# Kernel tuning notes

Measured on AMD Instinct MI355X. Metric: run time of the kernel, lower is better.

Reference implementation:

```python
import jax, jax.numpy as jnp
import numpy as np

B, S, C = 32, 128, 32
VOCAB, E, H = 262, 128, 256


def _gru_dir(x_proj, mask, W_hh, b_hh, reverse):
    # x_proj: [C, N, 3H] time-major precomputed input projection
    # mask:   [C, N, 1]  1.0 where char is valid
    N = x_proj.shape[1]
    h0 = jnp.zeros((N, H), x_proj.dtype)

    def step(h, inp):
        x3, mt = inp
        gh = h @ W_hh.T + b_hh                      # [N, 3H]
        hr, hz, hn = jnp.split(gh, 3, axis=-1)
        xr, xz, xn = jnp.split(x3, 3, axis=-1)
        r = jax.nn.sigmoid(xr + hr)
        z = jax.nn.sigmoid(xz + hz)
        n = jnp.tanh(xn + r * hn)
        hnew = (1.0 - z) * n + z * h
        h = mt * hnew + (1.0 - mt) * h              # freeze state past seq end
        return h, None

    hT, _ = jax.lax.scan(step, h0, (x_proj, mask), reverse=reverse)
    return hT  # [N, H] final state at last valid step (fw) / step 0 (bw)


def char_rnn_forward(chars, chars_mask, data_mask, embed,
                     W_ih_fw, W_hh_fw, b_ih_fw, b_hh_fw,
                     W_ih_bw, W_hh_bw, b_ih_bw, b_hh_bw):
    b, s, c = chars.shape
    N = b * s
    x = embed[chars.reshape(N, c)]                      # [N, C, E]
    m = chars_mask.reshape(N, c).astype(x.dtype)        # [N, C]
    mm = jnp.moveaxis(m, 1, 0)[:, :, None]              # [C, N, 1]

    def run(W_ih, b_ih, W_hh, b_hh, reverse):
        xp = jnp.einsum('nce,ge->ncg', x, W_ih) + b_ih  # [N, C, 3H]
        xp = jnp.moveaxis(xp, 1, 0)                     # [C, N, 3H]
        return _gru_dir(xp, mm, W_hh, b_hh, reverse)

    h_fw = run(W_ih_fw, b_ih_fw, W_hh_fw, b_hh_fw, False)
    h_bw = run(W_ih_bw, b_ih_bw, W_hh_bw, b_hh_bw, True)
    final = jnp.concatenate([h_fw, h_bw], axis=-1).reshape(b, s, 2 * H)
    return final * data_mask[:, :, None].astype(final.dtype)


def setup_inputs() -> dict:
    key = jax.random.key(0)
    ks = jax.random.split(key, 16)
    chars = jax.random.randint(ks[0], (B, S, C), 0, VOCAB, dtype=jnp.int32)
    # ragged but contiguous lengths, as pack_padded_sequence assumes (>=1)
    word_len = jax.random.randint(ks[1], (B,), 1, S + 1)
    char_len = jax.random.randint(ks[2], (B, S), 1, C + 1)
    data_mask = (jnp.arange(S)[None, :] < word_len[:, None]).astype(jnp.int32)
    chars_mask = (jnp.arange(C)[None, None, :] < char_len[:, :, None]).astype(jnp.int32)
    chars_mask = chars_mask * data_mask[:, :, None]
    # pack_padded needs length>=1 even for padded words (torch never runs them;
    # we mask their output with data_mask, so give them 1 valid char)
    chars_mask = chars_mask.at[:, :, 0].set(1)

    sc = 1.0 / np.sqrt(H)
    def unif(k, shape):
        return jax.random.uniform(k, shape, jnp.float32, -sc, sc)
    embed = jax.random.normal(ks[3], (VOCAB, E), jnp.float32) * 0.1
    return {
        'chars': chars, 'chars_mask': chars_mask, 'data_mask': data_mask,
        'embed': embed,
        'W_ih_fw': unif(ks[4], (3 * H, E)), 'W_hh_fw': unif(ks[5], (3 * H, H)),
        'b_ih_fw': unif(ks[6], (3 * H,)),  'b_hh_fw': unif(ks[7], (3 * H,)),
        'W_ih_bw': unif(ks[8], (3 * H, E)), 'W_hh_bw': unif(ks[9], (3 * H, H)),
        'b_ih_bw': unif(ks[10], (3 * H,)), 'b_hh_bw': unif(ks[11], (3 * H,)),
    }


def reference(chars, chars_mask, data_mask, embed,
              W_ih_fw, W_hh_fw, b_ih_fw, b_hh_fw,
              W_ih_bw, W_hh_bw, b_ih_bw, b_hh_bw):
    return char_rnn_forward(chars, chars_mask, data_mask, embed,
                            W_ih_fw, W_hh_fw, b_ih_fw, b_hh_fw,
                            W_ih_bw, W_hh_bw, b_ih_bw, b_hh_bw)
```

## Files before the change

kernel.cpp:

```cpp
#include <hip/hip_runtime.h>
#include <hip/hip_bf16.h>

typedef unsigned int u32;
typedef unsigned short u16;
typedef __attribute__((ext_vector_type(8))) short bf16x8;
typedef __attribute__((ext_vector_type(4))) float f32x4;

#define NWORDS 4096
#define CC 32
#define EE 128
#define HHH 256
#define MMW 32
#define VOCABN 262

#define HS 272
#define XPS 784

#define PK_HHD (16*3*8*512)
#define XP_OFF_U16 (2*PK_HHD)
#define XPD (VOCABN*768)
#define BIAS_OFF_U16 (XP_OFF_U16 + 2*XPD)

__device__ __forceinline__ float bf2f(u16 u){ union{u32 i; float f;} v; v.i=((u32)u)<<16; return v.f; }
__device__ __forceinline__ u16 f2bf(float f){
  __hip_bfloat16 h = __float2bfloat16(f);
  u16 r; __builtin_memcpy(&r, &h, 2); return r;
}
__device__ __forceinline__ float sigmoid_f(float x){
  float e = __builtin_amdgcn_exp2f(-1.4426950408889634f * x);
  return __builtin_amdgcn_rcpf(1.0f + e);
}
__device__ __forceinline__ float tanh_f(float x){
  float ax = __builtin_fabsf(x);
  float e  = __builtin_amdgcn_exp2f(-2.8853900817779268f * ax);
  float t  = 1.0f - 2.0f * e * __builtin_amdgcn_rcpf(1.0f + e);
  return __builtin_copysignf(t, x);
}

__global__ void prep_pack(const float* __restrict__ Whh_fw, const float* __restrict__ Whh_bw,
                          u16* __restrict__ wsu)
{
  int idx = blockIdx.x*256 + threadIdx.x;
  int d = idx / PK_HHD;
  int e = idx - d*PK_HHD;
  const float* Whh = d ? Whh_bw : Whh_fw;
  int jj   = e & 7;
  int lane = (e >> 3) & 63;
  int kc   = (e >> 9) & 7;
  int gnt  = e >> 12;
  int g = gnt % 3, nt = gnt / 3;
  int row = g*256 + nt*16 + (lane & 15);
  int k   = kc*32 + ((lane >> 4) << 3) + jj;
  wsu[idx] = f2bf(Whh[row*HHH + k]);
}

__global__ void prep_xp(const float* __restrict__ emb,
                        const float* __restrict__ Wih_fw, const float* __restrict__ Wih_bw,
                        u16* __restrict__ wsu)
{
  int i = blockIdx.x*256 + threadIdx.x;
  int d = i / XPD;
  int r = i - d*XPD;
  int c = r / 768, g = r - c*768;
  const float* W = (d ? Wih_bw : Wih_fw) + g*EE;
  const float* E = emb + c*EE;
  float acc = 0.0f;
  #pragma unroll 4
  for (int e = 0; e < EE; e += 4) {
    float4 ev = *(const float4*)(E + e);
    float4 wv = *(const float4*)(W + e);
    acc = fmaf(ev.w, wv.w, fmaf(ev.z, wv.z, fmaf(ev.y, wv.y, fmaf(ev.x, wv.x, acc))));
  }
  wsu[XP_OFF_U16 + i] = f2bf(acc);
}

__global__ void prep_bias(const float* __restrict__ bih_fw, const float* __restrict__ bhh_fw,
                          const float* __restrict__ bih_bw, const float* __restrict__ bhh_bw,
                          u16* __restrict__ wsu)
{
  int i = blockIdx.x*256 + threadIdx.x;
  if (i >= 2048) return;
  int d = i >> 10, o = i & 1023;
  const float* bih = d ? bih_bw : bih_fw;
  const float* bhh = d ? bhh_bw : bhh_fw;
  float v;
  if (o < 512)      v = bih[o] + bhh[o];
  else if (o < 768) v = bih[o - 512 + 512];
  else              v = bhh[o - 768 + 512];
  ((float*)(wsu + BIAS_OFF_U16))[d*1024 + o] = v;
}

__global__ __launch_bounds__(1024)
void gru_mfma(const int* __restrict__ chars, const int* __restrict__ chars_mask,
              const int* __restrict__ data_mask, const u16* __restrict__ wsu,
              float* __restrict__ out)
{
  const int dir   = blockIdx.x & 1;
  const int word0 = (blockIdx.x >> 1) * MMW;
  const int j     = threadIdx.x;
  const int wave  = j >> 6, lane = j & 63;
  const int quad  = lane >> 4, l15 = lane & 15;

  const bf16x8* pHH  = (const bf16x8*)(wsu + (size_t)dir*PK_HHD);
  const u16*    xpt  = wsu + XP_OFF_U16 + (size_t)dir*XPD;
  const float*  bias = (const float*)(wsu + BIAS_OFF_U16) + dir*1024;

  const bf16x8* bHH = pHH + (size_t)(wave*3)*8*64 + lane;

  __shared__ __align__(16) u16   sh_hhi[MMW][HS];
  __shared__ __align__(16) u16   sh_hlo[MMW][HS];
  __shared__ __align__(16) u16   sh_xp[MMW][XPS];
  __shared__ float sh_m[MMW];

  for (int i = j; i < MMW*HS/2; i += 1024) { ((float*)sh_hhi)[i] = 0.0f; ((float*)sh_hlo)[i] = 0.0f; }

  const int ch = wave*16 + l15;
  const float bR  = bias[ch],        bZ  = bias[256 + ch];
  const float bXN = bias[512 + ch],  bHN = bias[768 + ch];

  const int sw = j >> 5, sp = j & 31;

  bf16x8 buf[4][3];
  auto load_batch = [&](int kc, bf16x8 dst[3]) {
    #pragma unroll
    for (int g = 0; g < 3; ++g) dst[g] = bHH[(g*8 + kc)*64];
  };
  load_batch(0, buf[0]);
  load_batch(1, buf[1]);
  load_batch(2, buf[2]);

  #pragma unroll 1
  for (int s = 0; s < CC; ++s) {
    const int t = dir ? (CC - 1 - s) : s;
    __syncthreads();
    {
      int ci = chars[(word0 + sw)*CC + t];
      const uint4* src = (const uint4*)(xpt + (size_t)ci*768);
      uint4 a0 = src[sp*3], a1 = src[sp*3+1], a2 = src[sp*3+2];
      *(uint4*)&sh_xp[sw][sp*24]      = a0;
      *(uint4*)&sh_xp[sw][sp*24 + 8]  = a1;
      *(uint4*)&sh_xp[sw][sp*24 + 16] = a2;
      if (j < MMW) sh_m[j] = (float)chars_mask[(word0 + j)*CC + t];
    }
    __syncthreads();

    f32x4 acc[3][2];
    #pragma unroll
    for (int m = 0; m < 2; ++m) {
      acc[0][m] = (f32x4){bR,bR,bR,bR};
      acc[1][m] = (f32x4){bZ,bZ,bZ,bZ};
      acc[2][m] = (f32x4){bHN,bHN,bHN,bHN};
    }

    auto mfma_batch = [&](int kc, bf16x8 src[3]) {
      #pragma unroll
      for (int m = 0; m < 2; ++m) {
        bf16x8 ah = *(const bf16x8*)&sh_hhi[m*16 + l15][kc*32 + quad*8];
        bf16x8 al = *(const bf16x8*)&sh_hlo[m*16 + l15][kc*32 + quad*8];
        #pragma unroll
        for (int g = 0; g < 3; ++g) {
          const int ai = (g < 2) ? g : 2;
          acc[ai][m] = __builtin_amdgcn_mfma_f32_16x16x32_bf16(ah, src[g], acc[ai][m], 0,0,0);
          acc[ai][m] = __builtin_amdgcn_mfma_f32_16x16x32_bf16(al, src[g], acc[ai][m], 0,0,0);
        }
      }
    };

    #pragma unroll
    for (int b = 0; b < 8; ++b) {
      mfma_batch(b, buf[b & 3]);
      load_batch((b + 3) & 7, buf[(b + 3) & 3]);
    }

    __syncthreads();

    #pragma unroll
    for (int m = 0; m < 2; ++m)
      #pragma unroll
      for (int r = 0; r < 4; ++r) {
        const int word = m*16 + quad*4 + r;
        float xr = bf2f(sh_xp[word][ch]);
        float xz = bf2f(sh_xp[word][256 + ch]);
        float xn = bf2f(sh_xp[word][512 + ch]);
        float rr = sigmoid_f(acc[0][m][r] + xr);
        float zz = sigmoid_f(acc[1][m][r] + xz);
        float nn = tanh_f(fmaf(rr, acc[2][m][r], bXN + xn));
        float hold = bf2f(sh_hhi[word][ch]) + bf2f(sh_hlo[word][ch]);
        float hnew = fmaf(zz, hold - nn, nn);
        float hm   = fmaf(sh_m[word], hnew - hold, hold);
        u16 hi = f2bf(hm);
        sh_hhi[word][ch] = hi;
        sh_hlo[word][ch] = f2bf(hm - bf2f(hi));
      }
  }
  __syncthreads();

  const int oc = j & 255, og = j >> 8;
  #pragma unroll
  for (int i = 0; i < 8; ++i) {
    const int w = og*8 + i;
    float dm = (float)data_mask[word0 + w];
    float h = bf2f(sh_hhi[w][oc]) + bf2f(sh_hlo[w][oc]);
    out[(size_t)(word0 + w)*(2*HHH) + dir*HHH + oc] = h * dm;
  }
}

extern "C" void kernel_launch(void* const* d_in, const int* in_sizes, int n_in,
                              void* d_out, int out_size, void* d_ws, size_t ws_size,
                              hipStream_t stream) {
  const int*   chars      = (const int*)d_in[0];
  const int*   chars_mask = (const int*)d_in[1];
  const int*   data_mask  = (const int*)d_in[2];
  const float* embed      = (const float*)d_in[3];
  const float* Wih_fw     = (const float*)d_in[4];
  const float* Whh_fw     = (const float*)d_in[5];
  const float* bih_fw     = (const float*)d_in[6];
  const float* bhh_fw     = (const float*)d_in[7];
  const float* Wih_bw     = (const float*)d_in[8];
  const float* Whh_bw     = (const float*)d_in[9];
  const float* bih_bw     = (const float*)d_in[10];
  const float* bhh_bw     = (const float*)d_in[11];
  u16* wsu = (u16*)d_ws;

  prep_pack<<<2*PK_HHD/256, 256, 0, stream>>>(Whh_fw, Whh_bw, wsu);
  prep_xp<<<2*XPD/256, 256, 0, stream>>>(embed, Wih_fw, Wih_bw, wsu);
  prep_bias<<<8, 256, 0, stream>>>(bih_fw, bhh_fw, bih_bw, bhh_bw, wsu);

  gru_mfma<<<(NWORDS/MMW)*2, 1024, 0, stream>>>(chars, chars_mask, data_mask, wsu, (float*)d_out);
}
```

Baseline: 432.8 us.

## Double-buffer input projection gather, preload chars/masks, merge prep kernels

```diff
diff --git a/kernel.cpp b/kernel.cpp
--- a/kernel.cpp
+++ b/kernel.cpp
@@ -21,6 +21,11 @@
 #define XPD (VOCABN*768)
 #define BIAS_OFF_U16 (XP_OFF_U16 + 2*XPD)
 
+#define PREP_PACK_BLKS (2*PK_HHD/256)
+#define PREP_XP_BLKS   (2*XPD/256)
+#define PREP_BIAS_BLKS 8
+#define PREP_BLKS (PREP_PACK_BLKS + PREP_XP_BLKS + PREP_BIAS_BLKS)
+
 __device__ __forceinline__ float bf2f(u16 u){ union{u32 i; float f;} v; v.i=((u32)u)<<16; return v.f; }
 __device__ __forceinline__ u16 f2bf(float f){
   __hip_bfloat16 h = __float2bfloat16(f);
@@ -37,57 +42,54 @@
   return __builtin_copysignf(t, x);
 }
 
-__global__ void prep_pack(const float* __restrict__ Whh_fw, const float* __restrict__ Whh_bw,
-                          u16* __restrict__ wsu)
+__global__ void prep_all(const float* __restrict__ emb,
+                         const float* __restrict__ Wih_fw, const float* __restrict__ Whh_fw,
+                         const float* __restrict__ bih_fw, const float* __restrict__ bhh_fw,
+                         const float* __restrict__ Wih_bw, const float* __restrict__ Whh_bw,
+                         const float* __restrict__ bih_bw, const float* __restrict__ bhh_bw,
+                         u16* __restrict__ wsu)
 {
-  int idx = blockIdx.x*256 + threadIdx.x;
-  int d = idx / PK_HHD;
-  int e = idx - d*PK_HHD;
-  const float* Whh = d ? Whh_bw : Whh_fw;
-  int jj   = e & 7;
-  int lane = (e >> 3) & 63;
-  int kc   = (e >> 9) & 7;
-  int gnt  = e >> 12;
-  int g = gnt % 3, nt = gnt / 3;
-  int row = g*256 + nt*16 + (lane & 15);
-  int k   = kc*32 + ((lane >> 4) << 3) + jj;
-  wsu[idx] = f2bf(Whh[row*HHH + k]);
-}
-
-__global__ void prep_xp(const float* __restrict__ emb,
-                        const float* __restrict__ Wih_fw, const float* __restrict__ Wih_bw,
-                        u16* __restrict__ wsu)
-{
-  int i = blockIdx.x*256 + threadIdx.x;
-  int d = i / XPD;
-  int r = i - d*XPD;
-  int c = r / 768, g = r - c*768;
-  const float* W = (d ? Wih_bw : Wih_fw) + g*EE;
-  const float* E = emb + c*EE;
-  float acc = 0.0f;
-  #pragma unroll 4
-  for (int e = 0; e < EE; e += 4) {
-    float4 ev = *(const float4*)(E + e);
-    float4 wv = *(const float4*)(W + e);
-    acc = fmaf(ev.w, wv.w, fmaf(ev.z, wv.z, fmaf(ev.y, wv.y, fmaf(ev.x, wv.x, acc))));
-  }
-  wsu[XP_OFF_U16 + i] = f2bf(acc);
-}
-
-__global__ void prep_bias(const float* __restrict__ bih_fw, const float* __restrict__ bhh_fw,
-                          const float* __restrict__ bih_bw, const float* __restrict__ bhh_bw,
-                          u16* __restrict__ wsu)
-{
-  int i = blockIdx.x*256 + threadIdx.x;
-  if (i >= 2048) return;
-  int d = i >> 10, o = i & 1023;
-  const float* bih = d ? bih_bw : bih_fw;
-  const float* bhh = d ? bhh_bw : bhh_fw;
-  float v;
-  if (o < 512)      v = bih[o] + bhh[o];
-  else if (o < 768) v = bih[o - 512 + 512];
-  else              v = bhh[o - 768 + 512];
-  ((float*)(wsu + BIAS_OFF_U16))[d*1024 + o] = v;
+  const int bid = blockIdx.x, tid = threadIdx.x;
+  if (bid < PREP_PACK_BLKS) {
+    int idx = bid*256 + tid;
+    int d = idx / PK_HHD;
+    int e = idx - d*PK_HHD;
+    const float* Whh = d ? Whh_bw : Whh_fw;
+    int jj   = e & 7;
+    int lane = (e >> 3) & 63;
+    int kc   = (e >> 9) & 7;
+    int gnt  = e >> 12;
+    int g = gnt % 3, nt = gnt / 3;
+    int row = g*256 + nt*16 + (lane & 15);
+    int k   = kc*32 + ((lane >> 4) << 3) + jj;
+    wsu[idx] = f2bf(Whh[row*HHH + k]);
+  } else if (bid < PREP_PACK_BLKS + PREP_XP_BLKS) {
+    int i = (bid - PREP_PACK_BLKS)*256 + tid;
+    int d = i / XPD;
+    int r = i - d*XPD;
+    int c = r / 768, g = r - c*768;
+    const float* W = (d ? Wih_bw : Wih_fw) + g*EE;
+    const float* E = emb + c*EE;
+    float acc = 0.0f;
+    #pragma unroll 4
+    for (int e = 0; e < EE; e += 4) {
+      float4 ev = *(const float4*)(E + e);
+      float4 wv = *(const float4*)(W + e);
+      acc = fmaf(ev.w, wv.w, fmaf(ev.z, wv.z, fmaf(ev.y, wv.y, fmaf(ev.x, wv.x, acc))));
+    }
+    wsu[XP_OFF_U16 + i] = f2bf(acc);
+  } else {
+    int i = (bid - PREP_PACK_BLKS - PREP_XP_BLKS)*256 + tid;
+    if (i >= 2048) return;
+    int d = i >> 10, o = i & 1023;
+    const float* bih = d ? bih_bw : bih_fw;
+    const float* bhh = d ? bhh_bw : bhh_fw;
+    float v;
+    if (o < 512)      v = bih[o] + bhh[o];
+    else if (o < 768) v = bih[o - 512 + 512];
+    else              v = bhh[o - 768 + 512];
+    ((float*)(wsu + BIAS_OFF_U16))[d*1024 + o] = v;
+  }
 }
 
 __global__ __launch_bounds__(1024)
@@ -109,9 +111,15 @@
 
   __shared__ __align__(16) u16   sh_hhi[MMW][HS];
   __shared__ __align__(16) u16   sh_hlo[MMW][HS];
-  __shared__ __align__(16) u16   sh_xp[MMW][XPS];
-  __shared__ float sh_m[MMW];
-
+  __shared__ __align__(16) u16   sh_xp[2][MMW][XPS];
+  __shared__ int   sh_ci[MMW][CC + 1];
+  __shared__ float sh_cm[MMW][CC + 1];
+
+  if (j < MMW*CC) {
+    const int w = j >> 5, c = j & 31;
+    sh_ci[w][c] = chars[(word0 + w)*CC + c];
+    sh_cm[w][c] = (float)chars_mask[(word0 + w)*CC + c];
+  }
   for (int i = j; i < MMW*HS/2; i += 1024) { ((float*)sh_hhi)[i] = 0.0f; ((float*)sh_hlo)[i] = 0.0f; }
 
   const int ch = wave*16 + l15;
@@ -119,6 +127,17 @@
   const float bXN = bias[512 + ch],  bHN = bias[768 + ch];
 
   const int sw = j >> 5, sp = j & 31;
+
+  __syncthreads();
+
+  {
+    const int t0 = dir ? (CC - 1) : 0;
+    const uint4* src = (const uint4*)(xpt + (size_t)sh_ci[sw][t0]*768);
+    uint4 a0 = src[sp], a1 = src[sp + 32], a2 = src[sp + 64];
+    *(uint4*)&sh_xp[0][sw][sp*8]         = a0;
+    *(uint4*)&sh_xp[0][sw][(sp + 32)*8]  = a1;
+    *(uint4*)&sh_xp[0][sw][(sp + 64)*8]  = a2;
+  }
 
   bf16x8 buf[4][3];
   auto load_batch = [&](int kc, bf16x8 dst[3]) {
@@ -129,20 +148,19 @@
   load_batch(1, buf[1]);
   load_batch(2, buf[2]);
 
+  __syncthreads();
+
   #pragma unroll 1
   for (int s = 0; s < CC; ++s) {
-    const int t = dir ? (CC - 1 - s) : s;
-    __syncthreads();
-    {
-      int ci = chars[(word0 + sw)*CC + t];
-      const uint4* src = (const uint4*)(xpt + (size_t)ci*768);
-      uint4 a0 = src[sp*3], a1 = src[sp*3+1], a2 = src[sp*3+2];
-      *(uint4*)&sh_xp[sw][sp*24]      = a0;
-      *(uint4*)&sh_xp[sw][sp*24 + 8]  = a1;
-      *(uint4*)&sh_xp[sw][sp*24 + 16] = a2;
-      if (j < MMW) sh_m[j] = (float)chars_mask[(word0 + j)*CC + t];
-    }
-    __syncthreads();
+    const int cb = s & 1, nb = cb ^ 1;
+
+    uint4 px0, px1, px2;
+    const bool pf = (s + 1 < CC);
+    if (pf) {
+      const int t2 = dir ? (CC - 2 - s) : (s + 1);
+      const uint4* src = (const uint4*)(xpt + (size_t)sh_ci[sw][t2]*768);
+      px0 = src[sp]; px1 = src[sp + 32]; px2 = src[sp + 64];
+    }
 
     f32x4 acc[3][2];
     #pragma unroll
@@ -172,28 +190,36 @@
       load_batch((b + 3) & 7, buf[(b + 3) & 3]);
     }
 
+    if (pf) {
+      *(uint4*)&sh_xp[nb][sw][sp*8]        = px0;
+      *(uint4*)&sh_xp[nb][sw][(sp + 32)*8] = px1;
+      *(uint4*)&sh_xp[nb][sw][(sp + 64)*8] = px2;
+    }
+
     __syncthreads();
 
+    const int t = dir ? (CC - 1 - s) : s;
     #pragma unroll
     for (int m = 0; m < 2; ++m)
       #pragma unroll
       for (int r = 0; r < 4; ++r) {
         const int word = m*16 + quad*4 + r;
-        float xr = bf2f(sh_xp[word][ch]);
-        float xz = bf2f(sh_xp[word][256 + ch]);
-        float xn = bf2f(sh_xp[word][512 + ch]);
+        float xr = bf2f(sh_xp[cb][word][ch]);
+        float xz = bf2f(sh_xp[cb][word][256 + ch]);
+        float xn = bf2f(sh_xp[cb][word][512 + ch]);
         float rr = sigmoid_f(acc[0][m][r] + xr);
         float zz = sigmoid_f(acc[1][m][r] + xz);
         float nn = tanh_f(fmaf(rr, acc[2][m][r], bXN + xn));
         float hold = bf2f(sh_hhi[word][ch]) + bf2f(sh_hlo[word][ch]);
         float hnew = fmaf(zz, hold - nn, nn);
-        float hm   = fmaf(sh_m[word], hnew - hold, hold);
+        float hm   = fmaf(sh_cm[word][t], hnew - hold, hold);
         u16 hi = f2bf(hm);
         sh_hhi[word][ch] = hi;
         sh_hlo[word][ch] = f2bf(hm - bf2f(hi));
       }
-  }
-  __syncthreads();
+
+    __syncthreads();
+  }
 
   const int oc = j & 255, og = j >> 8;
   #pragma unroll
@@ -222,9 +248,8 @@
   const float* bhh_bw     = (const float*)d_in[11];
   u16* wsu = (u16*)d_ws;
 
-  prep_pack<<<2*PK_HHD/256, 256, 0, stream>>>(Whh_fw, Whh_bw, wsu);
-  prep_xp<<<2*XPD/256, 256, 0, stream>>>(embed, Wih_fw, Wih_bw, wsu);
-  prep_bias<<<8, 256, 0, stream>>>(bih_fw, bhh_fw, bih_bw, bhh_bw, wsu);
+  prep_all<<<PREP_BLKS, 256, 0, stream>>>(embed, Wih_fw, Whh_fw, bih_fw, bhh_fw,
+                                          Wih_bw, Whh_bw, bih_bw, bhh_bw, wsu);
 
   gru_mfma<<<(NWORDS/MMW)*2, 1024, 0, stream>>>(chars, chars_mask, data_mask, wsu, (float*)d_out);
 }
```

After: 619.3 us. 1.43x slower.
